# Performance work log

Measured on AMD Instinct MI355X. Metric: run time of the kernel, lower is better.

Reference implementation:

```python
import jax, jax.numpy as jnp
import numpy as np
import math

B, S, IN_DIM, OUT_DIM = 16, 1024, 512, 256
THETA = 10000.0


def _rope_single(x, cos, sin):
    # x: [B,S,D]; cos/sin: [D//2] -- SAME rotation applied at every position
    # (faithful to original: freqs_cis[seq_len*2] selects a single row)
    xr = x.reshape(x.shape[0], x.shape[1], -1, 2)
    a, b = xr[..., 0], xr[..., 1]
    out = jnp.stack([a * cos - b * sin, a * sin + b * cos], axis=-1)
    return out.reshape(x.shape)


def setup_inputs() -> dict:
    key = jax.random.key(0)
    ks = jax.random.split(key, 4)
    scale = 1.0 / math.sqrt(IN_DIM)
    x = jax.random.normal(ks[0], (B, S, IN_DIM), jnp.float32)
    wq = jax.random.normal(ks[1], (OUT_DIM, IN_DIM), jnp.float32) * scale
    wk = jax.random.normal(ks[2], (OUT_DIM, IN_DIM), jnp.float32) * scale
    wv = jax.random.normal(ks[3], (OUT_DIM, IN_DIM), jnp.float32) * scale
    bq = jnp.zeros((OUT_DIM,), jnp.float32)
    bk = jnp.zeros((OUT_DIM,), jnp.float32)
    bv = jnp.zeros((OUT_DIM,), jnp.float32)
    return {"x": x, "wq": wq, "bq": bq, "wk": wk, "bk": bk, "wv": wv, "bv": bv}


def reference(x, wq, bq, wk, bk, wv, bv):
    dim = x.shape[-1]  # scale uses INPUT dim, per original code
    # freqs_cis row at position index = 2*seq_len
    inv_freq = 1.0 / (THETA ** (jnp.arange(0, OUT_DIM, 2, dtype=jnp.float32) / OUT_DIM))
    angle = (2.0 * S) * inv_freq  # [OUT_DIM//2]
    cos, sin = jnp.cos(angle), jnp.sin(angle)

    q = jnp.einsum('bsi,oi->bso', x, wq) + bq
    k = jnp.einsum('bsi,oi->bso', x, wk) + bk
    v = jnp.einsum('bsi,oi->bso', x, wv) + bv

    q = _rope_single(q, cos, sin)
    k = _rope_single(k, cos, sin)

    scores = jnp.einsum('bqd,bkd->bqk', q, k) / jnp.sqrt(jnp.float32(dim))
    scores = jax.nn.softmax(scores.astype(jnp.float32), axis=-1)
    out = jnp.einsum('bqk,bkd->bqd', scores, v)
    return out
```

## Files before the change

kernel.cpp:

```cpp
#include <hip/hip_runtime.h>
#include <hip/hip_bf16.h>


typedef __attribute__((ext_vector_type(8))) short short8;
typedef __attribute__((ext_vector_type(4))) short short4v;
typedef __attribute__((ext_vector_type(4))) float f32x4;

#define GLL16(g, l)                                                            \
  __builtin_amdgcn_global_load_lds(                                            \
      (const __attribute__((address_space(1))) unsigned int*)(g),              \
      (__attribute__((address_space(3))) unsigned int*)(l), 16, 0, 0)

static __device__ __forceinline__ short f2bf(float f) {
  __hip_bfloat16 h = __float2bfloat16(f);
  return __builtin_bit_cast(short, h);
}

__global__ __launch_bounds__(256) void qkv_gemm(
    const float* __restrict__ x, const float* __restrict__ wq,
    const float* __restrict__ wk, const float* __restrict__ wv,
    const float* __restrict__ bq, const float* __restrict__ bk,
    const float* __restrict__ bv, short* __restrict__ qb,
    short* __restrict__ kb, short* __restrict__ vt) {
  __shared__ __align__(16) char smem[32768];
  const int bid = blockIdx.x;
  const int swz = (bid & 7) * 96 + (bid >> 3);
  const int mt = swz / 6, nt = swz % 6;
  const int tid = threadIdx.x;
  const int w = tid >> 6, lane = tid & 63;
  const int g = lane >> 4, c = lane & 15;
  const int wm = w >> 1, wn = w & 1;

  const float* wsel = (nt < 2) ? wq : (nt < 4) ? wk : wv;
  const int wro = (nt & 1) * 128;

  f32x4 acc[4][4];
  const f32x4 fzero = {0.f, 0.f, 0.f, 0.f};
#pragma unroll
  for (int mi = 0; mi < 4; mi++)
#pragma unroll
    for (int ni = 0; ni < 4; ni++) acc[mi][ni] = fzero;

  const int arow = tid >> 4;
  const int acol4 = tid & 15;
  const int achunk = acol4 >> 1, ahalf = (tid & 1) * 8;

  for (int kk = 0; kk < 8; ++kk) {
    __syncthreads();
    float4 xv[8], wv8[8];
#pragma unroll
    for (int j = 0; j < 8; j++) {
      int row = j * 16 + arow;
      xv[j] = *(const float4*)(x + (mt * 128 + row) * 512 + kk * 64 + acol4 * 4);
    }
#pragma unroll
    for (int j = 0; j < 8; j++) {
      int row = j * 16 + arow;
      wv8[j] = *(const float4*)(wsel + (wro + row) * 512 + kk * 64 + acol4 * 4);
    }
#pragma unroll
    for (int j = 0; j < 8; j++) {
      int row = j * 16 + arow;
      short4v s4;
      s4[0] = f2bf(xv[j].x); s4[1] = f2bf(xv[j].y);
      s4[2] = f2bf(xv[j].z); s4[3] = f2bf(xv[j].w);
      *(short4v*)(smem + row * 128 + ((achunk ^ (row & 7)) * 16) + ahalf) = s4;
      short4v t4;
      t4[0] = f2bf(wv8[j].x); t4[1] = f2bf(wv8[j].y);
      t4[2] = f2bf(wv8[j].z); t4[3] = f2bf(wv8[j].w);
      *(short4v*)(smem + 16384 + row * 128 + ((achunk ^ (row & 7)) * 16) + ahalf) = t4;
    }
    __syncthreads();
#pragma unroll
    for (int ks = 0; ks < 2; ++ks) {
      short8 af[4], bf[4];
#pragma unroll
      for (int mi = 0; mi < 4; mi++) {
        int row = wm * 64 + mi * 16 + c;
        af[mi] = *(const short8*)(smem + row * 128 + (((ks * 4 + g) ^ (row & 7)) * 16));
      }
#pragma unroll
      for (int ni = 0; ni < 4; ni++) {
        int row = wn * 64 + ni * 16 + c;
        bf[ni] = *(const short8*)(smem + 16384 + row * 128 + (((ks * 4 + g) ^ (row & 7)) * 16));
      }
#pragma unroll
      for (int mi = 0; mi < 4; mi++)
#pragma unroll
        for (int ni = 0; ni < 4; ni++)
          acc[mi][ni] = __builtin_amdgcn_mfma_f32_16x16x32_bf16(af[mi], bf[ni], acc[mi][ni], 0, 0, 0);
    }
  }

  const int cls = nt >> 1;
  const int cw = (nt & 1) * 128 + wn * 64;
  const int rowbase = mt * 128 + wm * 64;
  if (cls == 0) {
#pragma unroll
    for (int ni = 0; ni < 4; ni++) {
      int col = cw + ni * 16 + c;
      float bias = bq[col];
#pragma unroll
      for (int mi = 0; mi < 4; mi++)
#pragma unroll
        for (int j = 0; j < 4; j++) {
          int row = rowbase + mi * 16 + g * 4 + j;
          qb[row * 256 + col] = f2bf((acc[mi][ni][j] + bias) * 0.044194173824159216f);
        }
    }
  } else if (cls == 1) {
#pragma unroll
    for (int ni = 0; ni < 4; ni++) {
      int col = cw + ni * 16 + c;
      float bias = bk[col];
#pragma unroll
      for (int mi = 0; mi < 4; mi++)
#pragma unroll
        for (int j = 0; j < 4; j++) {
          int row = rowbase + mi * 16 + g * 4 + j;
          kb[row * 256 + col] = f2bf(acc[mi][ni][j] + bias);
        }
    }
  } else {
    __syncthreads();
    char* tb = smem + w * 8192;
#pragma unroll
    for (int ni = 0; ni < 4; ni++) {
      int dl = ni * 16 + c;
      float bias = bv[cw + dl];
#pragma unroll
      for (int mi = 0; mi < 4; mi++)
#pragma unroll
        for (int j = 0; j < 4; j++) {
          int sl = mi * 16 + g * 4 + j;
          *(short*)(tb + dl * 128 + ((sl * 2) ^ ((dl & 7) << 4))) =
              f2bf(acc[mi][ni][j] + bias);
        }
    }
    const int bb = rowbase >> 10, sb = rowbase & 1023;
#pragma unroll
    for (int i = 0; i < 8; i++) {
      int dl = i * 8 + (lane >> 3);
      int ch = lane & 7;
      short8 val = *(const short8*)(tb + dl * 128 + ((ch ^ (dl & 7)) * 16));
      *(short8*)(vt + (bb * 256 + cw + dl) * 1024 + sb + ch * 8) = val;
    }
  }
}

__global__ __launch_bounds__(512) void attn_kernel(
    const short* __restrict__ qb, const short* __restrict__ kb,
    const short* __restrict__ vt, float* __restrict__ out) {
  __shared__ __align__(16) char smem[149504];
  const int bid = blockIdx.x;
  const int swz = (bid & 7) * 32 + (bid >> 3);
  const int b = swz >> 4, qt = swz & 15;
  const int tid = threadIdx.x;
  const int w = tid >> 6, lane = tid & 63;
  const int grp = w >> 2, lw = w & 3;
  const int g = lane >> 4, c = lane & 15;
  const int q0 = b * 1024 + qt * 64 + lw * 16;
  char* kbase = smem + grp * 32768;
  char* vbase = smem + 65536 + grp * 32768;
  short* sp = (short*)(smem + 131072 + w * 2304);

  short8 qf[8];
#pragma unroll
  for (int ks = 0; ks < 8; ks++)
    qf[ks] = *(const short8*)(qb + (q0 + c) * 256 + ks * 32 + g * 8);

  f32x4 O[16];
  const f32x4 fzero = {0.f, 0.f, 0.f, 0.f};
#pragma unroll
  for (int ni = 0; ni < 16; ni++) O[ni] = fzero;
  float m_[4] = {-1e30f, -1e30f, -1e30f, -1e30f};
  float l_[4] = {0.f, 0.f, 0.f, 0.f};

  const int krow0 = b * 1024 + grp * 512;

  for (int kt = 0; kt < 8; ++kt) {
    __syncthreads();
    if (lw < 2) {
#pragma unroll
      for (int i = 0; i < 16; i++) {
        int j = lw * 16 + i;
        int r = j * 2 + (lane >> 5);
        int cc = lane & 31;
        GLL16(kb + (krow0 + kt * 64 + r) * 256 + ((cc ^ (r & 7)) * 8),
              kbase + j * 1024);
      }
    } else {
#pragma unroll
      for (int i = 0; i < 16; i++) {
        int j = (lw - 2) * 16 + i;
        int r = j * 8 + (lane >> 3);
        int cc = lane & 7;
        GLL16(vt + (b * 256 + r) * 1024 + grp * 512 + kt * 64 + ((cc ^ (r & 7)) * 8),
              vbase + j * 1024);
      }
    }
    asm volatile("s_waitcnt vmcnt(0)" ::: "memory");
    __syncthreads();

    f32x4 Sf[4];
#pragma unroll
    for (int nf = 0; nf < 4; nf++) Sf[nf] = fzero;
#pragma unroll
    for (int ks = 0; ks < 8; ks++) {
      short8 kf[4];
#pragma unroll
      for (int nf = 0; nf < 4; nf++) {
        int key = nf * 16 + c;
        kf[nf] = *(const short8*)(kbase + key * 512 + (((ks * 4 + g) ^ (c & 7)) * 16));
      }
#pragma unroll
      for (int nf = 0; nf < 4; nf++)
        Sf[nf] = __builtin_amdgcn_mfma_f32_16x16x32_bf16(qf[ks], kf[nf], Sf[nf], 0, 0, 0);
    }

    float Pv[4][4], scl[4];
#pragma unroll
    for (int j = 0; j < 4; j++) {
      float tm = fmaxf(fmaxf(Sf[0][j], Sf[1][j]), fmaxf(Sf[2][j], Sf[3][j]));
      tm = fmaxf(tm, __shfl_xor(tm, 1));
      tm = fmaxf(tm, __shfl_xor(tm, 2));
      tm = fmaxf(tm, __shfl_xor(tm, 4));
      tm = fmaxf(tm, __shfl_xor(tm, 8));
      float nm = fmaxf(m_[j], tm);
      scl[j] = __expf(m_[j] - nm);
      m_[j] = nm;
      float rs = 0.f;
#pragma unroll
      for (int nf = 0; nf < 4; nf++) {
        float p = __expf(Sf[nf][j] - nm);
        Pv[nf][j] = p;
        rs += p;
      }
      rs += __shfl_xor(rs, 1);
      rs += __shfl_xor(rs, 2);
      rs += __shfl_xor(rs, 4);
      rs += __shfl_xor(rs, 8);
      l_[j] = l_[j] * scl[j] + rs;
    }
#pragma unroll
    for (int ni = 0; ni < 16; ni++) {
      O[ni][0] *= scl[0]; O[ni][1] *= scl[1];
      O[ni][2] *= scl[2]; O[ni][3] *= scl[3];
    }

#pragma unroll
    for (int nf = 0; nf < 4; nf++)
#pragma unroll
      for (int j = 0; j < 4; j++)
        sp[(g * 4 + j) * 72 + nf * 16 + c] = f2bf(Pv[nf][j]);

    short8 pf[2];
#pragma unroll
    for (int ks2 = 0; ks2 < 2; ks2++)
      pf[ks2] = *(const short8*)((char*)sp + c * 144 + ks2 * 64 + g * 16);

#pragma unroll
    for (int ni = 0; ni < 16; ni++) {
      int d = ni * 16 + c;
#pragma unroll
      for (int ks2 = 0; ks2 < 2; ks2++) {
        short8 vf = *(const short8*)(vbase + d * 128 + (((ks2 * 4 + g) ^ (c & 7)) * 16));
        O[ni] = __builtin_amdgcn_mfma_f32_16x16x32_bf16(pf[ks2], vf, O[ni], 0, 0, 0);
      }
    }
  }

  __syncthreads();
  if (grp == 1) {
    char* ob = smem + lw * 20480;
#pragma unroll
    for (int ni = 0; ni < 16; ni++)
      *(f32x4*)(ob + (ni * 16 + c) * 80 + g * 16) = O[ni];
    float2* mlb = (float2*)(smem + 131072);
#pragma unroll
    for (int j = 0; j < 4; j++) {
      float2 ml; ml.x = m_[j]; ml.y = l_[j];
      mlb[lw * 16 + g * 4 + j] = ml;
    }
  }
  __syncthreads();
  if (grp == 0) {
    char* ob = smem + lw * 20480;
    const float2* mlb = (const float2*)(smem + 131072);
    float a1[4], a2[4], inv[4];
#pragma unroll
    for (int j = 0; j < 4; j++) {
      float2 ml2 = mlb[lw * 16 + g * 4 + j];
      float mm = fmaxf(m_[j], ml2.x);
      a1[j] = __expf(m_[j] - mm);
      a2[j] = __expf(ml2.x - mm);
      float l = a1[j] * l_[j] + a2[j] * ml2.y;
      inv[j] = 1.0f / l;
    }
#pragma unroll
    for (int ni = 0; ni < 16; ni++) {
      f32x4 o2 = *(const f32x4*)(ob + (ni * 16 + c) * 80 + g * 16);
#pragma unroll
      for (int j = 0; j < 4; j++) {
        int row = q0 + g * 4 + j;
        out[row * 256 + ni * 16 + c] = (a1[j] * O[ni][j] + a2[j] * o2[j]) * inv[j];
      }
    }
  }
}

extern "C" void kernel_launch(void* const* d_in, const int* in_sizes, int n_in,
                              void* d_out, int out_size, void* d_ws, size_t ws_size,
                              hipStream_t stream) {
  const float* x  = (const float*)d_in[0];
  const float* wq = (const float*)d_in[1];
  const float* bq = (const float*)d_in[2];
  const float* wk = (const float*)d_in[3];
  const float* bk = (const float*)d_in[4];
  const float* wv = (const float*)d_in[5];
  const float* bv = (const float*)d_in[6];
  float* out = (float*)d_out;
  char* ws = (char*)d_ws;
  short* qb = (short*)ws;
  short* kb = (short*)(ws + 8388608);
  short* vt = (short*)(ws + 16777216);

  qkv_gemm<<<768, 256, 0, stream>>>(x, wq, wk, wv, bq, bk, bv, qb, kb, vt);
  attn_kernel<<<256, 512, 0, stream>>>(qb, kb, vt, out);
}
```

Measured before the change: 156.3 us.

## Split attention keys across four wave groups, prefetch GEMM tiles, lazy rescale

The QKV GEMM now loads the next K-slice of x and weights into registers before the MFMA loop, so global loads overlap compute. The attention kernel moves to 1024 threads, with four key-split groups of 256 keys each and 32-key tiles per step. A four-way softmax merge runs through LDS in two halves. Online-softmax rescaling is skipped unless a row max grows by more than 8, which trades some exactness of the exp arguments for fewer rescales. Per-wave work per tile gets smaller and there are more barriers, and the 1024-thread block with 4 waves/SIMD raises register pressure risk.

```diff
diff --git a/kernel.cpp b/kernel.cpp
--- a/kernel.cpp
+++ b/kernel.cpp
@@ -45,19 +45,16 @@
   const int acol4 = tid & 15;
   const int achunk = acol4 >> 1, ahalf = (tid & 1) * 8;
 
+  float4 xv[8], wv8[8];
+#pragma unroll
+  for (int j = 0; j < 8; j++) {
+    int row = j * 16 + arow;
+    xv[j] = *(const float4*)(x + (mt * 128 + row) * 512 + acol4 * 4);
+    wv8[j] = *(const float4*)(wsel + (wro + row) * 512 + acol4 * 4);
+  }
+
   for (int kk = 0; kk < 8; ++kk) {
     __syncthreads();
-    float4 xv[8], wv8[8];
-#pragma unroll
-    for (int j = 0; j < 8; j++) {
-      int row = j * 16 + arow;
-      xv[j] = *(const float4*)(x + (mt * 128 + row) * 512 + kk * 64 + acol4 * 4);
-    }
-#pragma unroll
-    for (int j = 0; j < 8; j++) {
-      int row = j * 16 + arow;
-      wv8[j] = *(const float4*)(wsel + (wro + row) * 512 + kk * 64 + acol4 * 4);
-    }
 #pragma unroll
     for (int j = 0; j < 8; j++) {
       int row = j * 16 + arow;
@@ -71,6 +68,14 @@
       *(short4v*)(smem + 16384 + row * 128 + ((achunk ^ (row & 7)) * 16) + ahalf) = t4;
     }
     __syncthreads();
+    if (kk < 7) {
+#pragma unroll
+      for (int j = 0; j < 8; j++) {
+        int row = j * 16 + arow;
+        xv[j] = *(const float4*)(x + (mt * 128 + row) * 512 + (kk + 1) * 64 + acol4 * 4);
+        wv8[j] = *(const float4*)(wsel + (wro + row) * 512 + (kk + 1) * 64 + acol4 * 4);
+      }
+    }
 #pragma unroll
     for (int ks = 0; ks < 2; ++ks) {
       short8 af[4], bf[4];
@@ -148,10 +153,10 @@
   }
 }
 
-__global__ __launch_bounds__(512) void attn_kernel(
+__global__ __launch_bounds__(1024, 4) void attn_kernel(
     const short* __restrict__ qb, const short* __restrict__ kb,
     const short* __restrict__ vt, float* __restrict__ out) {
-  __shared__ __align__(16) char smem[149504];
+  __shared__ __align__(16) char smem[153088];
   const int bid = blockIdx.x;
   const int swz = (bid & 7) * 32 + (bid >> 3);
   const int b = swz >> 4, qt = swz & 15;
@@ -160,9 +165,9 @@
   const int grp = w >> 2, lw = w & 3;
   const int g = lane >> 4, c = lane & 15;
   const int q0 = b * 1024 + qt * 64 + lw * 16;
-  char* kbase = smem + grp * 32768;
-  char* vbase = smem + 65536 + grp * 32768;
-  short* sp = (short*)(smem + 131072 + w * 2304);
+  char* kbase = smem + grp * 16384;
+  char* vbase = smem + 65536 + grp * 16384;
+  short* sp = (short*)(smem + 131072 + w * 1280);
 
   short8 qf[8];
 #pragma unroll
@@ -176,135 +181,188 @@
   float m_[4] = {-1e30f, -1e30f, -1e30f, -1e30f};
   float l_[4] = {0.f, 0.f, 0.f, 0.f};
 
-  const int krow0 = b * 1024 + grp * 512;
+  const int krow0 = b * 1024 + grp * 256;
 
   for (int kt = 0; kt < 8; ++kt) {
     __syncthreads();
-    if (lw < 2) {
-#pragma unroll
-      for (int i = 0; i < 16; i++) {
-        int j = lw * 16 + i;
-        int r = j * 2 + (lane >> 5);
-        int cc = lane & 31;
-        GLL16(kb + (krow0 + kt * 64 + r) * 256 + ((cc ^ (r & 7)) * 8),
-              kbase + j * 1024);
+#pragma unroll
+    for (int i = 0; i < 4; i++) {
+      int j = lw * 4 + i;
+      int r = j * 2 + (lane >> 5);
+      int cc = lane & 31;
+      GLL16(kb + (krow0 + kt * 32 + r) * 256 + ((cc ^ (r & 7)) * 8),
+            kbase + j * 1024);
+    }
+#pragma unroll
+    for (int i = 0; i < 4; i++) {
+      int j = lw * 4 + i;
+      int r = j * 16 + (lane >> 2);
+      int cc = lane & 3;
+      GLL16(vt + (b * 256 + r) * 1024 + grp * 256 + kt * 32 + ((cc ^ (r & 3)) * 8),
+            vbase + j * 1024);
+    }
+    asm volatile("s_waitcnt vmcnt(0)" ::: "memory");
+    __syncthreads();
+
+    f32x4 Sf[2];
+    Sf[0] = fzero; Sf[1] = fzero;
+#pragma unroll
+    for (int ks = 0; ks < 8; ks++) {
+      short8 kf[2];
+#pragma unroll
+      for (int nf = 0; nf < 2; nf++) {
+        int key = nf * 16 + c;
+        kf[nf] = *(const short8*)(kbase + key * 512 + (((ks * 4 + g) ^ (key & 7)) * 16));
+      }
+#pragma unroll
+      for (int nf = 0; nf < 2; nf++)
+        Sf[nf] = __builtin_amdgcn_mfma_f32_16x16x32_bf16(qf[ks], kf[nf], Sf[nf], 0, 0, 0);
+    }
+
+    float tm[4];
+#pragma unroll
+    for (int j = 0; j < 4; j++) {
+      float t = fmaxf(Sf[0][j], Sf[1][j]);
+      t = fmaxf(t, __shfl_xor(t, 1));
+      t = fmaxf(t, __shfl_xor(t, 2));
+      t = fmaxf(t, __shfl_xor(t, 4));
+      t = fmaxf(t, __shfl_xor(t, 8));
+      tm[j] = t;
+    }
+    bool need = (tm[0] > m_[0] + 8.f) || (tm[1] > m_[1] + 8.f) ||
+                (tm[2] > m_[2] + 8.f) || (tm[3] > m_[3] + 8.f);
+    float Pv[2][4];
+    if (__any(need)) {
+      float scl[4];
+#pragma unroll
+      for (int j = 0; j < 4; j++) {
+        float nm = fmaxf(m_[j], tm[j]);
+        scl[j] = __expf(m_[j] - nm);
+        m_[j] = nm;
+        float rs = 0.f;
+#pragma unroll
+        for (int nf = 0; nf < 2; nf++) {
+          float p = __expf(Sf[nf][j] - nm);
+          Pv[nf][j] = p;
+          rs += p;
+        }
+        rs += __shfl_xor(rs, 1);
+        rs += __shfl_xor(rs, 2);
+        rs += __shfl_xor(rs, 4);
+        rs += __shfl_xor(rs, 8);
+        l_[j] = l_[j] * scl[j] + rs;
+      }
+#pragma unroll
+      for (int ni = 0; ni < 16; ni++) {
+        O[ni][0] *= scl[0]; O[ni][1] *= scl[1];
+        O[ni][2] *= scl[2]; O[ni][3] *= scl[3];
       }
     } else {
 #pragma unroll
-      for (int i = 0; i < 16; i++) {
-        int j = (lw - 2) * 16 + i;
-        int r = j * 8 + (lane >> 3);
-        int cc = lane & 7;
-        GLL16(vt + (b * 256 + r) * 1024 + grp * 512 + kt * 64 + ((cc ^ (r & 7)) * 8),
-              vbase + j * 1024);
-      }
-    }
-    asm volatile("s_waitcnt vmcnt(0)" ::: "memory");
-    __syncthreads();
-
-    f32x4 Sf[4];
-#pragma unroll
-    for (int nf = 0; nf < 4; nf++) Sf[nf] = fzero;
-#pragma unroll
-    for (int ks = 0; ks < 8; ks++) {
-      short8 kf[4];
-#pragma unroll
-      for (int nf = 0; nf < 4; nf++) {
-        int key = nf * 16 + c;
-        kf[nf] = *(const short8*)(kbase + key * 512 + (((ks * 4 + g) ^ (c & 7)) * 16));
-      }
-#pragma unroll
-      for (int nf = 0; nf < 4; nf++)
-        Sf[nf] = __builtin_amdgcn_mfma_f32_16x16x32_bf16(qf[ks], kf[nf], Sf[nf], 0, 0, 0);
-    }
-
-    float Pv[4][4], scl[4];
-#pragma unroll
-    for (int j = 0; j < 4; j++) {
-      float tm = fmaxf(fmaxf(Sf[0][j], Sf[1][j]), fmaxf(Sf[2][j], Sf[3][j]));
-      tm = fmaxf(tm, __shfl_xor(tm, 1));
-      tm = fmaxf(tm, __shfl_xor(tm, 2));
-      tm = fmaxf(tm, __shfl_xor(tm, 4));
-      tm = fmaxf(tm, __shfl_xor(tm, 8));
-      float nm = fmaxf(m_[j], tm);
-      scl[j] = __expf(m_[j] - nm);
-      m_[j] = nm;
-      float rs = 0.f;
-#pragma unroll
-      for (int nf = 0; nf < 4; nf++) {
-        float p = __expf(Sf[nf][j] - nm);
-        Pv[nf][j] = p;
-        rs += p;
-      }
-      rs += __shfl_xor(rs, 1);
-      rs += __shfl_xor(rs, 2);
-      rs += __shfl_xor(rs, 4);
-      rs += __shfl_xor(rs, 8);
-      l_[j] = l_[j] * scl[j] + rs;
-    }
-#pragma unroll
-    for (int ni = 0; ni < 16; ni++) {
-      O[ni][0] *= scl[0]; O[ni][1] *= scl[1];
-      O[ni][2] *= scl[2]; O[ni][3] *= scl[3];
-    }
-
-#pragma unroll
-    for (int nf = 0; nf < 4; nf++)
+      for (int j = 0; j < 4; j++) {
+        float rs = 0.f;
+#pragma unroll
+        for (int nf = 0; nf < 2; nf++) {
+          float p = __expf(Sf[nf][j] - m_[j]);
+          Pv[nf][j] = p;
+          rs += p;
+        }
+        rs += __shfl_xor(rs, 1);
+        rs += __shfl_xor(rs, 2);
+        rs += __shfl_xor(rs, 4);
+        rs += __shfl_xor(rs, 8);
+        l_[j] += rs;
+      }
+    }
+
+#pragma unroll
+    for (int nf = 0; nf < 2; nf++)
 #pragma unroll
       for (int j = 0; j < 4; j++)
-        sp[(g * 4 + j) * 72 + nf * 16 + c] = f2bf(Pv[nf][j]);
-
-    short8 pf[2];
-#pragma unroll
-    for (int ks2 = 0; ks2 < 2; ks2++)
-      pf[ks2] = *(const short8*)((char*)sp + c * 144 + ks2 * 64 + g * 16);
+        sp[(g * 4 + j) * 40 + nf * 16 + c] = f2bf(Pv[nf][j]);
+
+    short8 pf = *(const short8*)((char*)sp + c * 80 + g * 16);
 
 #pragma unroll
     for (int ni = 0; ni < 16; ni++) {
       int d = ni * 16 + c;
-#pragma unroll
-      for (int ks2 = 0; ks2 < 2; ks2++) {
-        short8 vf = *(const short8*)(vbase + d * 128 + (((ks2 * 4 + g) ^ (c & 7)) * 16));
-        O[ni] = __builtin_amdgcn_mfma_f32_16x16x32_bf16(pf[ks2], vf, O[ni], 0, 0, 0);
-      }
+      short8 vf = *(const short8*)(vbase + d * 64 + ((g ^ (d & 3)) * 16));
+      O[ni] = __builtin_amdgcn_mfma_f32_16x16x32_bf16(pf, vf, O[ni], 0, 0, 0);
     }
   }
 
   __syncthreads();
-  if (grp == 1) {
-    char* ob = smem + lw * 20480;
-#pragma unroll
-    for (int ni = 0; ni < 16; ni++)
-      *(f32x4*)(ob + (ni * 16 + c) * 80 + g * 16) = O[ni];
-    float2* mlb = (float2*)(smem + 131072);
+  float2* mlb = (float2*)(smem + 151552);
+  if (grp != 0) {
+    char* reg0 = smem + ((grp - 1) * 4 + lw) * 8192;
+#pragma unroll
+    for (int ni = 0; ni < 8; ni++)
+      *(f32x4*)(reg0 + ni * 1024 + c * 64 + g * 16) = O[ni];
 #pragma unroll
     for (int j = 0; j < 4; j++) {
       float2 ml; ml.x = m_[j]; ml.y = l_[j];
-      mlb[lw * 16 + g * 4 + j] = ml;
-    }
+      mlb[((grp - 1) * 4 + lw) * 16 + g * 4 + j] = ml;
+    }
+  }
+  __syncthreads();
+  float as[3][4], inv[4];
+  if (grp == 0) {
+    float mm[4];
+    float2 mls[3][4];
+#pragma unroll
+    for (int j = 0; j < 4; j++) {
+      mm[j] = m_[j];
+#pragma unroll
+      for (int s = 0; s < 3; s++) {
+        mls[s][j] = mlb[(s * 4 + lw) * 16 + g * 4 + j];
+        mm[j] = fmaxf(mm[j], mls[s][j].x);
+      }
+      float a0 = __expf(m_[j] - mm[j]);
+      float lsum = a0 * l_[j];
+#pragma unroll
+      for (int s = 0; s < 3; s++) {
+        as[s][j] = __expf(mls[s][j].x - mm[j]);
+        lsum += as[s][j] * mls[s][j].y;
+      }
+      inv[j] = 1.0f / lsum;
+#pragma unroll
+      for (int ni = 0; ni < 16; ni++) O[ni][j] *= a0;
+    }
+#pragma unroll
+    for (int ni = 0; ni < 8; ni++) {
+      f32x4 acc2 = O[ni];
+#pragma unroll
+      for (int s = 0; s < 3; s++) {
+        f32x4 o2 = *(const f32x4*)(smem + (s * 4 + lw) * 8192 + ni * 1024 + c * 64 + g * 16);
+        acc2[0] += as[s][0] * o2[0]; acc2[1] += as[s][1] * o2[1];
+        acc2[2] += as[s][2] * o2[2]; acc2[3] += as[s][3] * o2[3];
+      }
+#pragma unroll
+      for (int j = 0; j < 4; j++)
+        out[(q0 + g * 4 + j) * 256 + ni * 16 + c] = acc2[j] * inv[j];
+    }
+  }
+  __syncthreads();
+  if (grp != 0) {
+    char* reg0 = smem + ((grp - 1) * 4 + lw) * 8192;
+#pragma unroll
+    for (int ni = 8; ni < 16; ni++)
+      *(f32x4*)(reg0 + (ni - 8) * 1024 + c * 64 + g * 16) = O[ni];
   }
   __syncthreads();
   if (grp == 0) {
-    char* ob = smem + lw * 20480;
-    const float2* mlb = (const float2*)(smem + 131072);
-    float a1[4], a2[4], inv[4];
-#pragma unroll
-    for (int j = 0; j < 4; j++) {
-      float2 ml2 = mlb[lw * 16 + g * 4 + j];
-      float mm = fmaxf(m_[j], ml2.x);
-      a1[j] = __expf(m_[j] - mm);
-      a2[j] = __expf(ml2.x - mm);
-      float l = a1[j] * l_[j] + a2[j] * ml2.y;
-      inv[j] = 1.0f / l;
-    }
-#pragma unroll
-    for (int ni = 0; ni < 16; ni++) {
-      f32x4 o2 = *(const f32x4*)(ob + (ni * 16 + c) * 80 + g * 16);
-#pragma unroll
-      for (int j = 0; j < 4; j++) {
-        int row = q0 + g * 4 + j;
-        out[row * 256 + ni * 16 + c] = (a1[j] * O[ni][j] + a2[j] * o2[j]) * inv[j];
-      }
+#pragma unroll
+    for (int ni = 8; ni < 16; ni++) {
+      f32x4 acc2 = O[ni];
+#pragma unroll
+      for (int s = 0; s < 3; s++) {
+        f32x4 o2 = *(const f32x4*)(smem + (s * 4 + lw) * 8192 + (ni - 8) * 1024 + c * 64 + g * 16);
+        acc2[0] += as[s][0] * o2[0]; acc2[1] += as[s][1] * o2[1];
+        acc2[2] += as[s][2] * o2[2]; acc2[3] += as[s][3] * o2[3];
+      }
+#pragma unroll
+      for (int j = 0; j < 4; j++)
+        out[(q0 + g * 4 + j) * 256 + ni * 16 + c] = acc2[j] * inv[j];
     }
   }
 }
@@ -326,5 +384,5 @@
   short* vt = (short*)(ws + 16777216);
 
   qkv_gemm<<<768, 256, 0, stream>>>(x, wq, wk, wv, bq, bk, bv, qb, kb, vt);
-  attn_kernel<<<256, 512, 0, stream>>>(qb, kb, vt, out);
+  attn_kernel<<<256, 1024, 0, stream>>>(qb, kb, vt, out);
 }
```

Measured after the change: 382.0 us. 144% more time.
